# Performance work log

Hardware: AMD Instinct MI355X
Metric: run time of the kernel (lower is better)

Reference implementation:

```python
import jax, jax.numpy as jnp
import numpy as np

D_MODEL = 512
TOP_K = 4


def setup_inputs() -> dict:
    key = jax.random.key(0)
    ks = jax.random.split(key, 7)
    B, L, D = 16, 2048, D_MODEL
    s = 1.0 / np.sqrt(D)
    return {
        "x": jax.random.normal(ks[0], (B, L, D), dtype=jnp.float32),
        "Wq": jax.random.uniform(ks[1], (D, D), jnp.float32, -s, s),
        "bq": jax.random.uniform(ks[2], (D,), jnp.float32, -s, s),
        "Wk": jax.random.uniform(ks[3], (D, D), jnp.float32, -s, s),
        "bk": jax.random.uniform(ks[4], (D,), jnp.float32, -s, s),
        "Wv": jax.random.uniform(ks[5], (D, D), jnp.float32, -s, s),
        "bv": jax.random.uniform(ks[6], (D,), jnp.float32, -s, s),
    }


def reference(x, Wq, bq, Wk, bk, Wv, bv):
    B, L, D = x.shape
    # Linear projections (torch Linear: x @ W.T + b)
    Q = jnp.einsum('bld,ed->ble', x, Wq) + bq
    K = jnp.einsum('bld,ed->ble', x, Wk) + bk
    V = jnp.einsum('bld,ed->ble', x, Wv) + bv
    # FFT autocorrelation along time axis
    q_fft = jnp.fft.rfft(Q, axis=1)
    k_fft = jnp.fft.rfft(K, axis=1)
    corr = jnp.fft.irfft(q_fft * jnp.conj(k_fft), n=L, axis=1)  # [B, L, D]
    mean_corr = corr.mean(axis=-1)                               # [B, L]
    topk_vals, topk_idx = jax.lax.top_k(mean_corr, TOP_K)        # [B, K]
    weights = jax.nn.softmax(topk_vals, axis=-1)                 # [B, K]
    # torch.roll(V[b], shifts=lag, dims=0): out[t] = V[b, (t - lag) % L]
    t = jnp.arange(L)
    gather_idx = (t[None, None, :] - topk_idx[:, :, None]) % L   # [B, K, L]
    rolled = V[jnp.arange(B)[:, None, None], gather_idx]         # [B, K, L, D]
    agg = jnp.einsum('bk,bkld->bld', weights, rolled)
    return agg
```

## Files before the change

kernel.cpp:

```cpp
#include <hip/hip_runtime.h>
#include <math.h>

typedef unsigned short u16;
typedef unsigned int   u32;
typedef __attribute__((ext_vector_type(8))) __bf16 bf16x8;
typedef __attribute__((ext_vector_type(4))) float  f32x4;

#define BB 16
#define LL 2048
#define DD 512
#define NF 1025
#define TOPK 4

static const size_t OFF_XB  = 0;
static const size_t OFF_XTB = OFF_XB  + 8388608;
static const size_t OFF_GTB = OFF_XTB + 8388608;
static const size_t OFF_XC  = OFF_GTB + 8388608;
static const size_t OFF_BBM = OFF_XC  + 8388608;
static const size_t OFF_S   = OFF_BBM + 262144;
static const size_t OFF_W   = OFF_S   + (size_t)BB * NF * 2;
static const size_t OFF_I   = OFF_W   + BB * TOPK;

__device__ __forceinline__ u16 f2bf(float f) {
    u32 u = __float_as_uint(f);
    return (u16)((u + 0x7fffu + ((u >> 16) & 1u)) >> 16);
}
__device__ __forceinline__ float bf2f(u16 h) {
    return __uint_as_float(((u32)h) << 16);
}
__device__ __forceinline__ void gload16(const void* g, void* l) {
    __builtin_amdgcn_global_load_lds((const __attribute__((address_space(1))) void*)g,
                                     (__attribute__((address_space(3))) void*)l, 16, 0, 0);
}
__device__ __forceinline__ float2 cmul(float2 u, float2 v) {
    return make_float2(u.x * v.x - u.y * v.y, u.x * v.y + u.y * v.x);
}
__device__ __forceinline__ float2 cadd(float2 u, float2 v) { return make_float2(u.x + v.x, u.y + v.y); }
__device__ __forceinline__ float2 csub(float2 u, float2 v) { return make_float2(u.x - v.x, u.y - v.y); }

template<int M, int SGN>
__device__ __forceinline__ void radix4(const float2* __restrict__ src,
                                       float2* __restrict__ dst,
                                       const float2* __restrict__ twl, int tid) {
#pragma unroll
    for (int r = 0; r < 2; r++) {
        int w = tid + 256 * r;
        int k = w & (M - 1);
        int jm = w - k;
        float2 a = src[w], b = src[w + 512], c = src[w + 1024], d = src[w + 1536];
        float2 t0 = cadd(a, c), t1 = csub(a, c), t2 = cadd(b, d), bd = csub(b, d);
        float2 t3 = (SGN > 0) ? make_float2(bd.y, -bd.x)
                              : make_float2(-bd.y, bd.x);
        float2 T1 = twl[jm];
        float2 T2 = cmul(T1, T1);
        float2 T3 = cmul(T1, T2);
        int o = 4 * jm + k;
        dst[o]         = cadd(t0, t2);
        dst[o + M]     = cmul(cadd(t1, t3), T1);
        dst[o + 2 * M] = cmul(csub(t0, t2), T2);
        dst[o + 3 * M] = cmul(csub(t1, t3), T3);
    }
}

template<int SGN>
__device__ __forceinline__ void fft_r4_chain(float2* __restrict__ b1, float2* __restrict__ b2,
                                             const float2* __restrict__ twl, int tid) {
    radix4<2,   SGN>(b1, b2, twl, tid); __syncthreads();
    radix4<8,   SGN>(b2, b1, twl, tid); __syncthreads();
    radix4<32,  SGN>(b1, b2, twl, tid); __syncthreads();
    radix4<128, SGN>(b2, b1, twl, tid); __syncthreads();
    radix4<512, SGN>(b1, b2, twl, tid); __syncthreads();
}

__global__ __launch_bounds__(256) void k_pre(const float* __restrict__ x,
                                             const float* __restrict__ Wq,
                                             const float* __restrict__ Wk,
                                             const float* __restrict__ Wv,
                                             u16* __restrict__ xb,
                                             u16* __restrict__ xtb,
                                             u16* __restrict__ Bm,
                                             float* __restrict__ S) {
    __shared__ char sh[9216];
    int bid = blockIdx.x;
    int tid = threadIdx.x;
    if (bid < 64) {
        int g = bid;
        float (*As)[68] = (float(*)[68])sh;
        float (*Bs)[68] = (float(*)[68])(sh + 4352);
        int tx = tid & 15, ty = tid >> 4;
        int m0 = (g & 7) * 64, n0 = (g >> 3) * 64;
        float acc[4][4] = {};
        for (int k0 = 0; k0 < DD; k0 += 16) {
#pragma unroll
            for (int r = 0; r < 4; r++) {
                As[ty][tx + 16 * r] = Wq[(size_t)(k0 + ty) * DD + m0 + tx + 16 * r];
                Bs[ty][tx + 16 * r] = Wk[(size_t)(k0 + ty) * DD + n0 + tx + 16 * r];
            }
            __syncthreads();
#pragma unroll
            for (int k = 0; k < 16; k++) {
                float4 a4 = *(const float4*)&As[k][ty * 4];
                float4 b4 = *(const float4*)&Bs[k][tx * 4];
                float a[4] = {a4.x, a4.y, a4.z, a4.w};
                float b[4] = {b4.x, b4.y, b4.z, b4.w};
#pragma unroll
                for (int i = 0; i < 4; i++)
#pragma unroll
                    for (int j = 0; j < 4; j++) acc[i][j] += a[i] * b[j];
            }
            __syncthreads();
        }
#pragma unroll
        for (int i = 0; i < 4; i++) {
            uint2 o;
            o.x = (u32)f2bf(acc[i][0]) | ((u32)f2bf(acc[i][1]) << 16);
            o.y = (u32)f2bf(acc[i][2]) | ((u32)f2bf(acc[i][3]) << 16);
            *(uint2*)&Bm[(size_t)(m0 + ty * 4 + i) * DD + n0 + tx * 4] = o;
        }
    } else if (bid < 320) {
        int g = bid - 64;
        int i4 = g * 256 + tid;
        float4 w = ((const float4*)Wv)[i4];
        ushort4 o;
        o.x = f2bf(w.x); o.y = f2bf(w.y); o.z = f2bf(w.z); o.w = f2bf(w.w);
        ((ushort4*)(Bm + DD * DD))[i4] = o;
        if (i4 < 8200)
            ((float4*)S)[i4] = make_float4(0.f, 0.f, 0.f, 0.f);
    } else {
        int tb = bid - 320;
        int bx = tb & 7;
        int by = (tb >> 3) & 31;
        int bz = tb >> 8;
        u16 (*tile)[72] = (u16(*)[72])sh;
        int tx = tid & 15, ty = tid >> 4;
        int d0 = bx * 64, t0 = by * 64;
        const float* ip = x + ((size_t)bz * LL + t0) * DD + d0;
        u16* xbp = xb + ((size_t)bz * LL + t0) * DD + d0;
#pragma unroll
        for (int i = 0; i < 4; i++) {
            int r = ty + 16 * i;
            float4 v = *(const float4*)&ip[(size_t)r * DD + tx * 4];
            uint2 o;
            o.x = (u32)f2bf(v.x) | ((u32)f2bf(v.y) << 16);
            o.y = (u32)f2bf(v.z) | ((u32)f2bf(v.w) << 16);
            *(uint2*)&xbp[(size_t)r * DD + tx * 4] = o;
            tile[tx * 4 + 0][r] = (u16)(o.x);
            tile[tx * 4 + 1][r] = (u16)(o.x >> 16);
            tile[tx * 4 + 2][r] = (u16)(o.y);
            tile[tx * 4 + 3][r] = (u16)(o.y >> 16);
        }
        __syncthreads();
        u16* xtp = xtb + ((size_t)bz * DD + d0) * LL + t0;
#pragma unroll
        for (int i = 0; i < 2; i++) {
            int idx = tid + 256 * i;
            int dr = idx >> 3;
            int ch = idx & 7;
            uint4 o = *(const uint4*)&tile[dr][ch * 8];
            *(uint4*)&xtp[(size_t)dr * LL + ch * 8] = o;
        }
    }
}

__global__ __launch_bounds__(256, 2) void k_gemm2(const u16* __restrict__ Ab,
                                                  const u16* __restrict__ Bm,
                                                  u16* __restrict__ GTB) {
    __shared__ u16 smem[16384];
    u16* As = smem;
    u16* Bs = smem + 8192;
    int t = threadIdx.x;
    int wave = t >> 6, lane = t & 63;
    int l15 = lane & 15, l4 = lane >> 4;
    int qr = wave & 1, qc = wave >> 1;
    int m0 = blockIdx.x * 128, n0 = blockIdx.y * 128;

    f32x4 acc[4][4];
#pragma unroll
    for (int i = 0; i < 4; i++)
#pragma unroll
        for (int j = 0; j < 4; j++) acc[i][j] = (f32x4){0.f, 0.f, 0.f, 0.f};

    const u16* Ag = Ab + (size_t)m0 * DD;
    const u16* Bg = Bm + (size_t)n0 * DD;
    int a_base = (qr * 64 + l15) * 64 + l4 * 8;
    int b_base = (qc * 64 + l15) * 64 + l4 * 8;

    for (int k0 = 0; k0 < DD; k0 += 64) {
#pragma unroll
        for (int n = 0; n < 4; n++) {
            int c = wave * 256 + n * 64 + lane;
            int row = c >> 3, col = (c & 7) * 8;
            gload16(Ag + (size_t)row * DD + k0 + col, (char*)As + (size_t)(wave * 256 + n * 64) * 16);
            gload16(Bg + (size_t)row * DD + k0 + col, (char*)Bs + (size_t)(wave * 256 + n * 64) * 16);
        }
        __syncthreads();
#pragma unroll
        for (int kk = 0; kk < 64; kk += 32) {
            bf16x8 af[4], bq[4];
#pragma unroll
            for (int i = 0; i < 4; i++) af[i] = *(const bf16x8*)(As + a_base + i * 1024 + kk);
#pragma unroll
            for (int j = 0; j < 4; j++) bq[j] = *(const bf16x8*)(Bs + b_base + j * 1024 + kk);
#pragma unroll
            for (int i = 0; i < 4; i++)
#pragma unroll
                for (int j = 0; j < 4; j++)
                    acc[i][j] = __builtin_amdgcn_mfma_f32_16x16x32_bf16(af[i], bq[j], acc[i][j], 0, 0, 0);
        }
        __syncthreads();
    }

    float4* tb4 = (float4*)smem;
    int bidx = m0 >> 11;
    int tbase = m0 & 2047;
#pragma unroll
    for (int p = 0; p < 2; p++) {
        __syncthreads();
        if (qc == p) {
#pragma unroll
            for (int j = 0; j < 4; j++) {
                int nloc = j * 16 + l15;
#pragma unroll
                for (int i = 0; i < 4; i++) {
                    int tq = qr * 16 + i * 4 + l4;
                    tb4[nloc * 32 + (tq ^ (nloc & 31))] = *(float4*)&acc[i][j];
                }
            }
        }
        __syncthreads();
#pragma unroll
        for (int u = 0; u < 8; u++) {
            int idx4 = u * 256 + t;
            int nloc = idx4 >> 5, c4 = idx4 & 31;
            float4 v = tb4[nloc * 32 + (c4 ^ (nloc & 31))];
            uint2 o;
            o.x = (u32)f2bf(v.x) | ((u32)f2bf(v.y) << 16);
            o.y = (u32)f2bf(v.z) | ((u32)f2bf(v.w) << 16);
            *(uint2*)&GTB[((size_t)bidx * DD + n0 + p * 64 + nloc) * LL + tbase + c4 * 4] = o;
        }
    }
}

__global__ __launch_bounds__(256, 2) void k_gemm3(const u16* __restrict__ Ab,
                                                  const u16* __restrict__ Bm,
                                                  const float* __restrict__ bv,
                                                  float* __restrict__ out) {
    __shared__ u16 smem[16384];
    u16* As = smem;
    u16* Bs = smem + 8192;
    int t = threadIdx.x;
    int wave = t >> 6, lane = t & 63;
    int l15 = lane & 15, l4 = lane >> 4;
    int qr = wave & 1, qc = wave >> 1;
    int m0 = blockIdx.x * 128, n0 = blockIdx.y * 128;

    f32x4 acc[4][4];
#pragma unroll
    for (int i = 0; i < 4; i++)
#pragma unroll
        for (int j = 0; j < 4; j++) acc[i][j] = (f32x4){0.f, 0.f, 0.f, 0.f};

    const u16* Ag = Ab + (size_t)m0 * DD;
    const u16* Bg = Bm + (size_t)DD * DD + (size_t)n0 * DD;
    int a_base = (qr * 64 + l15) * 64 + l4 * 8;
    int b_base = (qc * 64 + l15) * 64 + l4 * 8;

    for (int k0 = 0; k0 < DD; k0 += 64) {
#pragma unroll
        for (int n = 0; n < 4; n++) {
            int c = wave * 256 + n * 64 + lane;
            int row = c >> 3, col = (c & 7) * 8;
            gload16(Ag + (size_t)row * DD + k0 + col, (char*)As + (size_t)(wave * 256 + n * 64) * 16);
            gload16(Bg + (size_t)row * DD + k0 + col, (char*)Bs + (size_t)(wave * 256 + n * 64) * 16);
        }
        __syncthreads();
#pragma unroll
        for (int kk = 0; kk < 64; kk += 32) {
            bf16x8 af[4], bq[4];
#pragma unroll
            for (int i = 0; i < 4; i++) af[i] = *(const bf16x8*)(As + a_base + i * 1024 + kk);
#pragma unroll
            for (int j = 0; j < 4; j++) bq[j] = *(const bf16x8*)(Bs + b_base + j * 1024 + kk);
#pragma unroll
            for (int i = 0; i < 4; i++)
#pragma unroll
                for (int j = 0; j < 4; j++)
                    acc[i][j] = __builtin_amdgcn_mfma_f32_16x16x32_bf16(af[i], bq[j], acc[i][j], 0, 0, 0);
        }
        __syncthreads();
    }

    float*  tb  = (float*)smem;
    float4* tb4 = (float4*)smem;
#pragma unroll
    for (int p = 0; p < 2; p++) {
        __syncthreads();
        if (qr == p) {
#pragma unroll
            for (int j = 0; j < 4; j++) {
                int nloc = qc * 64 + j * 16 + l15;
#pragma unroll
                for (int i = 0; i < 4; i++) {
#pragma unroll
                    for (int r = 0; r < 4; r++) {
                        int mloc = i * 16 + l4 * 4 + r;
                        int nc = ((nloc >> 2) ^ (mloc & 31)) << 2;
                        tb[mloc * 128 + nc + (nloc & 3)] = acc[i][j][r];
                    }
                }
            }
        }
        __syncthreads();
#pragma unroll
        for (int u = 0; u < 8; u++) {
            int idx4 = u * 256 + t;
            int mloc = idx4 >> 5, c4 = idx4 & 31;
            float4 v = tb4[mloc * 32 + (c4 ^ (mloc & 31))];
            float4 bias = *(const float4*)&bv[n0 + c4 * 4];
            v.x += bias.x; v.y += bias.y; v.z += bias.z; v.w += bias.w;
            *(float4*)&out[(size_t)(m0 + p * 64 + mloc) * DD + n0 + c4 * 4] = v;
        }
    }
}

__global__ __launch_bounds__(256) void k_fft(const u16* __restrict__ XTB,
                                             const u16* __restrict__ GTB,
                                             float* __restrict__ S) {
    __shared__ float2 lds[5120];
    float2* b1  = lds;
    float2* b2  = lds + 2048;
    float2* twl = lds + 4096;
    int tid = threadIdx.x;
    int grp = blockIdx.x;
    int b = blockIdx.y;
    for (int j = tid; j < 1024; j += 256) {
        float sn, cs;
        sincosf(-6.283185307179586f * (float)j / 2048.0f, &sn, &cs);
        twl[j] = make_float2(cs, sn);
    }
    __syncthreads();
    float2 sr[4];
#pragma unroll
    for (int r = 0; r < 4; r++) sr[r] = make_float2(0.f, 0.f);
    float2 s1024 = make_float2(0.f, 0.f);

    for (int c = 0; c < 8; c++) {
        int d = grp * 8 + c;
        const u16* xp = XTB + ((size_t)b * DD + d) * LL;
        const u16* gp = GTB + ((size_t)b * DD + d) * LL;
#pragma unroll
        for (int h = 0; h < 2; h++) {
            int j0 = 2 * tid + 512 * h;
            u32 xl = *(const u32*)&xp[j0];
            u32 xh = *(const u32*)&xp[j0 + 1024];
            u32 gl = *(const u32*)&gp[j0];
            u32 gh = *(const u32*)&gp[j0 + 1024];
            float2 a0 = make_float2(bf2f((u16)xl), bf2f((u16)gl));
            float2 a1 = make_float2(bf2f((u16)(xl >> 16)), bf2f((u16)(gl >> 16)));
            float2 c0 = make_float2(bf2f((u16)xh), bf2f((u16)gh));
            float2 c1 = make_float2(bf2f((u16)(xh >> 16)), bf2f((u16)(gh >> 16)));
            b1[2 * j0]     = cadd(a0, c0);
            b1[2 * j0 + 1] = cmul(csub(a0, c0), twl[j0]);
            b1[2 * j0 + 2] = cadd(a1, c1);
            b1[2 * j0 + 3] = cmul(csub(a1, c1), twl[j0 + 1]);
        }
        __syncthreads();
        fft_r4_chain<1>(b1, b2, twl, tid);
#pragma unroll
        for (int r = 0; r < 4; r++) {
            int f = tid + 256 * r;
            float2 p = b2[f];
            float2 q = b2[(2048 - f) & 2047];
            float ar = 0.5f * (p.x + q.x), ai = 0.5f * (p.y - q.y);
            float dr = p.x - q.x, di = p.y + q.y;
            float gr = 0.5f * di, gi = -0.5f * dr;
            sr[r].x += ar * gr + ai * gi;
            sr[r].y += ai * gr - ar * gi;
        }
        if (tid == 0) {
            float2 p = b2[1024];
            s1024.x += p.x * p.y;
        }
    }
    float* Sg = S + (size_t)b * NF * 2;
#pragma unroll
    for (int r = 0; r < 4; r++) {
        int f = tid + 256 * r;
        atomicAdd(&Sg[2 * f], sr[r].x);
        atomicAdd(&Sg[2 * f + 1], sr[r].y);
    }
    if (tid == 0) {
        atomicAdd(&Sg[2048], s1024.x);
        atomicAdd(&Sg[2049], s1024.y);
    }
}

__global__ __launch_bounds__(256) void k_topk(const float* __restrict__ S,
                                              float* __restrict__ wts,
                                              int* __restrict__ idxs) {
    __shared__ float2 lds[5120];
    float2* b1  = lds;
    float2* b2  = lds + 2048;
    float2* twl = lds + 4096;
    __shared__ float cv[2048];
    __shared__ float rv[256];
    __shared__ int ri[256];
    __shared__ float topv[TOPK];
    __shared__ int topi[TOPK];
    int tid = threadIdx.x;
    int b = blockIdx.x;
    const float* Sg = S + (size_t)b * NF * 2;
    for (int j = tid; j < 1024; j += 256) {
        float sn, cs;
        sincosf(6.283185307179586f * (float)j / 2048.0f, &sn, &cs);
        twl[j] = make_float2(cs, sn);
    }
    __syncthreads();
#pragma unroll
    for (int h = 0; h < 2; h++) {
        int j0 = 2 * tid + 512 * h;
#pragma unroll
        for (int e = 0; e < 2; e++) {
            int j = j0 + e;
            float2 zl = make_float2(Sg[2 * j], Sg[2 * j + 1]);
            int fh = j + 1024;
            int ms = 2048 - fh;
            float2 zh = (fh == 1024) ? make_float2(Sg[2048], Sg[2049])
                                     : make_float2(Sg[2 * ms], -Sg[2 * ms + 1]);
            b1[2 * j]     = cadd(zl, zh);
            b1[2 * j + 1] = cmul(csub(zl, zh), twl[j]);
        }
    }
    __syncthreads();
    fft_r4_chain<-1>(b1, b2, twl, tid);
    const float scale = 1.0f / ((float)LL * (float)DD);
    for (int f = tid; f < 2048; f += 256) cv[f] = b2[f].x * scale;
    __syncthreads();
    for (int r = 0; r < TOPK; r++) {
        float best = -3.0e38f;
        int bi = 0x7fffffff;
        for (int f = tid; f < 2048; f += 256) {
            bool taken = false;
            for (int q = 0; q < r; q++) taken |= (topi[q] == f);
            float v = cv[f];
            if (!taken && (v > best || (v == best && f < bi))) { best = v; bi = f; }
        }
        rv[tid] = best; ri[tid] = bi;
        __syncthreads();
        for (int s = 128; s > 0; s >>= 1) {
            if (tid < s) {
                float v2 = rv[tid + s]; int i2 = ri[tid + s];
                if (v2 > rv[tid] || (v2 == rv[tid] && i2 < ri[tid])) { rv[tid] = v2; ri[tid] = i2; }
            }
            __syncthreads();
        }
        if (tid == 0) { topv[r] = rv[0]; topi[r] = ri[0]; }
        __syncthreads();
    }
    if (tid == 0) {
        float mx = topv[0];
        float e[TOPK], sum = 0.f;
        for (int k = 0; k < TOPK; k++) { e[k] = expf(topv[k] - mx); sum += e[k]; }
        for (int k = 0; k < TOPK; k++) {
            wts[b * TOPK + k] = e[k] / sum;
            idxs[b * TOPK + k] = topi[k];
        }
    }
}

__global__ __launch_bounds__(128) void k_combine(const u16* __restrict__ XB,
                                                 const float* __restrict__ wts,
                                                 const int* __restrict__ idxs,
                                                 u16* __restrict__ XC) {
    int l = blockIdx.x, b = blockIdx.y;
    int t = threadIdx.x;
    const ushort4* Xb = (const ushort4*)(XB + (size_t)b * LL * DD);
    float4 acc = make_float4(0.f, 0.f, 0.f, 0.f);
#pragma unroll
    for (int k = 0; k < TOPK; k++) {
        float w = wts[b * TOPK + k];
        int r = (l - idxs[b * TOPK + k]) & (LL - 1);
        ushort4 v = Xb[(size_t)r * 128 + t];
        acc.x += w * bf2f(v.x); acc.y += w * bf2f(v.y);
        acc.z += w * bf2f(v.z); acc.w += w * bf2f(v.w);
    }
    ushort4 o;
    o.x = f2bf(acc.x); o.y = f2bf(acc.y); o.z = f2bf(acc.z); o.w = f2bf(acc.w);
    ((ushort4*)(XC + (size_t)b * LL * DD))[(size_t)l * 128 + t] = o;
}

extern "C" void kernel_launch(void* const* d_in, const int* in_sizes, int n_in,
                              void* d_out, int out_size, void* d_ws, size_t ws_size,
                              hipStream_t stream) {
    const float* x  = (const float*)d_in[0];
    const float* Wq = (const float*)d_in[1];
    const float* Wk = (const float*)d_in[3];
    const float* Wv = (const float*)d_in[5];
    const float* bv = (const float*)d_in[6];
    (void)in_sizes; (void)n_in; (void)out_size; (void)ws_size;

    float* ws  = (float*)d_ws;
    u16*   XB  = (u16*)(ws + OFF_XB);
    u16*   XTB = (u16*)(ws + OFF_XTB);
    u16*   GTB = (u16*)(ws + OFF_GTB);
    u16*   XC  = (u16*)(ws + OFF_XC);
    u16*   BM  = (u16*)(ws + OFF_BBM);
    float* S   = ws + OFF_S;
    float* wts = ws + OFF_W;
    int*   idx = (int*)(ws + OFF_I);
    float* out = (float*)d_out;

    k_pre<<<4416, 256, 0, stream>>>(x, Wq, Wk, Wv, XB, XTB, BM, S);
    k_gemm2<<<dim3((BB * LL) / 128, DD / 128), 256, 0, stream>>>(XB, BM, GTB);
    k_fft<<<dim3(64, BB), 256, 0, stream>>>(XTB, GTB, S);
    k_topk<<<BB, 256, 0, stream>>>(S, wts, idx);
    k_combine<<<dim3(LL, BB), 128, 0, stream>>>(XB, wts, idx, XC);
    k_gemm3<<<dim3((BB * LL) / 128, DD / 128), 256, 0, stream>>>(XC, BM, bv, out);
}
```

Baseline: 314.9 us.

## Pad FFT LDS buffers and keep per-stage twiddles in registers

Adds a padding index P(i)=i+i/32 to every LDS access in the radix-4 FFT stages to cut bank conflicts. It drops the shared twiddle table, instead computing per-thread, per-stage twiddles once into registers with sincosf, and skips the trivial twiddle multiplies in the last stage. The first butterfly pass is reorganized around wider uint2 loads with contiguous writes, and k_fft gets a launch bound asking for 4 blocks per CU. The cost is more registers and extra sincosf calls per thread.

```diff
diff --git a/kernel.cpp b/kernel.cpp
--- a/kernel.cpp
+++ b/kernel.cpp
@@ -38,38 +38,64 @@
 __device__ __forceinline__ float2 cadd(float2 u, float2 v) { return make_float2(u.x + v.x, u.y + v.y); }
 __device__ __forceinline__ float2 csub(float2 u, float2 v) { return make_float2(u.x - v.x, u.y - v.y); }
 
+__device__ __forceinline__ int P(int i) { return i + (i >> 5); }
+
 template<int M, int SGN>
 __device__ __forceinline__ void radix4(const float2* __restrict__ src,
                                        float2* __restrict__ dst,
-                                       const float2* __restrict__ twl, int tid) {
+                                       const float2* __restrict__ tw, int tid) {
 #pragma unroll
     for (int r = 0; r < 2; r++) {
         int w = tid + 256 * r;
         int k = w & (M - 1);
         int jm = w - k;
-        float2 a = src[w], b = src[w + 512], c = src[w + 1024], d = src[w + 1536];
+        float2 a = src[P(w)], b = src[P(w + 512)], c = src[P(w + 1024)], d = src[P(w + 1536)];
         float2 t0 = cadd(a, c), t1 = csub(a, c), t2 = cadd(b, d), bd = csub(b, d);
         float2 t3 = (SGN > 0) ? make_float2(bd.y, -bd.x)
                               : make_float2(-bd.y, bd.x);
-        float2 T1 = twl[jm];
-        float2 T2 = cmul(T1, T1);
-        float2 T3 = cmul(T1, T2);
         int o = 4 * jm + k;
-        dst[o]         = cadd(t0, t2);
-        dst[o + M]     = cmul(cadd(t1, t3), T1);
-        dst[o + 2 * M] = cmul(csub(t0, t2), T2);
-        dst[o + 3 * M] = cmul(csub(t1, t3), T3);
+        if (M == 512) {
+            dst[P(o)]         = cadd(t0, t2);
+            dst[P(o + M)]     = cadd(t1, t3);
+            dst[P(o + 2 * M)] = csub(t0, t2);
+            dst[P(o + 3 * M)] = csub(t1, t3);
+        } else {
+            float2 T1 = tw[r];
+            float2 T2 = cmul(T1, T1);
+            float2 T3 = cmul(T1, T2);
+            dst[P(o)]         = cadd(t0, t2);
+            dst[P(o + M)]     = cmul(cadd(t1, t3), T1);
+            dst[P(o + 2 * M)] = cmul(csub(t0, t2), T2);
+            dst[P(o + 3 * M)] = cmul(csub(t1, t3), T3);
+        }
     }
 }
 
 template<int SGN>
 __device__ __forceinline__ void fft_r4_chain(float2* __restrict__ b1, float2* __restrict__ b2,
-                                             const float2* __restrict__ twl, int tid) {
-    radix4<2,   SGN>(b1, b2, twl, tid); __syncthreads();
-    radix4<8,   SGN>(b2, b1, twl, tid); __syncthreads();
-    radix4<32,  SGN>(b1, b2, twl, tid); __syncthreads();
-    radix4<128, SGN>(b2, b1, twl, tid); __syncthreads();
-    radix4<512, SGN>(b1, b2, twl, tid); __syncthreads();
+                                             const float2 (*tws)[2], int tid) {
+    radix4<2,   SGN>(b1, b2, tws[0], tid); __syncthreads();
+    radix4<8,   SGN>(b2, b1, tws[1], tid); __syncthreads();
+    radix4<32,  SGN>(b1, b2, tws[2], tid); __syncthreads();
+    radix4<128, SGN>(b2, b1, tws[3], tid); __syncthreads();
+    radix4<512, SGN>(b1, b2, tws[4], tid); __syncthreads();
+}
+
+template<int SGN>
+__device__ __forceinline__ void make_tw(float2 tws[5][2], int tid) {
+    const float sc = (SGN > 0 ? -6.283185307179586f : 6.283185307179586f) / 2048.0f;
+#pragma unroll
+    for (int st = 0; st < 5; st++) {
+        int M = 2 << (2 * st);
+#pragma unroll
+        for (int r = 0; r < 2; r++) {
+            int w = tid + 256 * r;
+            int jm = w - (w & (M - 1));
+            float sn, cs;
+            sincosf(sc * (float)jm, &sn, &cs);
+            tws[st][r] = make_float2(cs, sn);
+        }
+    }
 }
 
 __global__ __launch_bounds__(256) void k_pre(const float* __restrict__ x,
@@ -323,54 +349,58 @@
     }
 }
 
-__global__ __launch_bounds__(256) void k_fft(const u16* __restrict__ XTB,
-                                             const u16* __restrict__ GTB,
-                                             float* __restrict__ S) {
-    __shared__ float2 lds[5120];
-    float2* b1  = lds;
-    float2* b2  = lds + 2048;
-    float2* twl = lds + 4096;
+__global__ __launch_bounds__(256, 4) void k_fft(const u16* __restrict__ XTB,
+                                                const u16* __restrict__ GTB,
+                                                float* __restrict__ S) {
+    __shared__ float2 lds[4224];
+    float2* b1 = lds;
+    float2* b2 = lds + 2112;
     int tid = threadIdx.x;
     int grp = blockIdx.x;
     int b = blockIdx.y;
-    for (int j = tid; j < 1024; j += 256) {
+
+    float2 tws[5][2];
+    make_tw<1>(tws, tid);
+    float2 tw2[4];
+#pragma unroll
+    for (int e = 0; e < 4; e++) {
         float sn, cs;
-        sincosf(-6.283185307179586f * (float)j / 2048.0f, &sn, &cs);
-        twl[j] = make_float2(cs, sn);
-    }
-    __syncthreads();
+        sincosf(-6.283185307179586f / 2048.0f * (float)(4 * tid + e), &sn, &cs);
+        tw2[e] = make_float2(cs, sn);
+    }
+
     float2 sr[4];
 #pragma unroll
     for (int r = 0; r < 4; r++) sr[r] = make_float2(0.f, 0.f);
-    float2 s1024 = make_float2(0.f, 0.f);
+    float s1024 = 0.f;
 
     for (int c = 0; c < 8; c++) {
         int d = grp * 8 + c;
         const u16* xp = XTB + ((size_t)b * DD + d) * LL;
         const u16* gp = GTB + ((size_t)b * DD + d) * LL;
-#pragma unroll
-        for (int h = 0; h < 2; h++) {
-            int j0 = 2 * tid + 512 * h;
-            u32 xl = *(const u32*)&xp[j0];
-            u32 xh = *(const u32*)&xp[j0 + 1024];
-            u32 gl = *(const u32*)&gp[j0];
-            u32 gh = *(const u32*)&gp[j0 + 1024];
-            float2 a0 = make_float2(bf2f((u16)xl), bf2f((u16)gl));
-            float2 a1 = make_float2(bf2f((u16)(xl >> 16)), bf2f((u16)(gl >> 16)));
-            float2 c0 = make_float2(bf2f((u16)xh), bf2f((u16)gh));
-            float2 c1 = make_float2(bf2f((u16)(xh >> 16)), bf2f((u16)(gh >> 16)));
-            b1[2 * j0]     = cadd(a0, c0);
-            b1[2 * j0 + 1] = cmul(csub(a0, c0), twl[j0]);
-            b1[2 * j0 + 2] = cadd(a1, c1);
-            b1[2 * j0 + 3] = cmul(csub(a1, c1), twl[j0 + 1]);
-        }
-        __syncthreads();
-        fft_r4_chain<1>(b1, b2, twl, tid);
+        int j0 = 4 * tid;
+        uint2 xl = *(const uint2*)&xp[j0];
+        uint2 xh = *(const uint2*)&xp[j0 + 1024];
+        uint2 gl = *(const uint2*)&gp[j0];
+        uint2 gh = *(const uint2*)&gp[j0 + 1024];
+        u32 xlw[2] = {xl.x, xl.y}, xhw[2] = {xh.x, xh.y};
+        u32 glw[2] = {gl.x, gl.y}, ghw[2] = {gh.x, gh.y};
+        float2* wp = &b1[P(8 * tid)];
+#pragma unroll
+        for (int e = 0; e < 4; e++) {
+            int sh = 16 * (e & 1);
+            float2 a0 = make_float2(bf2f((u16)(xlw[e >> 1] >> sh)), bf2f((u16)(glw[e >> 1] >> sh)));
+            float2 c0 = make_float2(bf2f((u16)(xhw[e >> 1] >> sh)), bf2f((u16)(ghw[e >> 1] >> sh)));
+            wp[2 * e]     = cadd(a0, c0);
+            wp[2 * e + 1] = cmul(csub(a0, c0), tw2[e]);
+        }
+        __syncthreads();
+        fft_r4_chain<1>(b1, b2, tws, tid);
 #pragma unroll
         for (int r = 0; r < 4; r++) {
             int f = tid + 256 * r;
-            float2 p = b2[f];
-            float2 q = b2[(2048 - f) & 2047];
+            float2 p = b2[P(f)];
+            float2 q = b2[P((2048 - f) & 2047)];
             float ar = 0.5f * (p.x + q.x), ai = 0.5f * (p.y - q.y);
             float dr = p.x - q.x, di = p.y + q.y;
             float gr = 0.5f * di, gi = -0.5f * dr;
@@ -378,8 +408,8 @@
             sr[r].y += ai * gr - ar * gi;
         }
         if (tid == 0) {
-            float2 p = b2[1024];
-            s1024.x += p.x * p.y;
+            float2 p = b2[P(1024)];
+            s1024 += p.x * p.y;
         }
     }
     float* Sg = S + (size_t)b * NF * 2;
@@ -390,18 +420,16 @@
         atomicAdd(&Sg[2 * f + 1], sr[r].y);
     }
     if (tid == 0) {
-        atomicAdd(&Sg[2048], s1024.x);
-        atomicAdd(&Sg[2049], s1024.y);
+        atomicAdd(&Sg[2048], s1024);
     }
 }
 
 __global__ __launch_bounds__(256) void k_topk(const float* __restrict__ S,
                                               float* __restrict__ wts,
                                               int* __restrict__ idxs) {
-    __shared__ float2 lds[5120];
-    float2* b1  = lds;
-    float2* b2  = lds + 2048;
-    float2* twl = lds + 4096;
+    __shared__ float2 lds[4224];
+    float2* b1 = lds;
+    float2* b2 = lds + 2112;
     __shared__ float cv[2048];
     __shared__ float rv[256];
     __shared__ int ri[256];
@@ -410,31 +438,31 @@
     int tid = threadIdx.x;
     int b = blockIdx.x;
     const float* Sg = S + (size_t)b * NF * 2;
-    for (int j = tid; j < 1024; j += 256) {
-        float sn, cs;
-        sincosf(6.283185307179586f * (float)j / 2048.0f, &sn, &cs);
-        twl[j] = make_float2(cs, sn);
-    }
-    __syncthreads();
+
+    float2 tws[5][2];
+    make_tw<-1>(tws, tid);
+
 #pragma unroll
     for (int h = 0; h < 2; h++) {
-        int j0 = 2 * tid + 512 * h;
 #pragma unroll
         for (int e = 0; e < 2; e++) {
-            int j = j0 + e;
+            int j = 2 * tid + 512 * h + e;
+            float sn, cs;
+            sincosf(6.283185307179586f / 2048.0f * (float)j, &sn, &cs);
+            float2 T = make_float2(cs, sn);
             float2 zl = make_float2(Sg[2 * j], Sg[2 * j + 1]);
             int fh = j + 1024;
             int ms = 2048 - fh;
             float2 zh = (fh == 1024) ? make_float2(Sg[2048], Sg[2049])
                                      : make_float2(Sg[2 * ms], -Sg[2 * ms + 1]);
-            b1[2 * j]     = cadd(zl, zh);
-            b1[2 * j + 1] = cmul(csub(zl, zh), twl[j]);
+            b1[P(2 * j)]     = cadd(zl, zh);
+            b1[P(2 * j + 1)] = cmul(csub(zl, zh), T);
         }
     }
     __syncthreads();
-    fft_r4_chain<-1>(b1, b2, twl, tid);
+    fft_r4_chain<-1>(b1, b2, tws, tid);
     const float scale = 1.0f / ((float)LL * (float)DD);
-    for (int f = tid; f < 2048; f += 256) cv[f] = b2[f].x * scale;
+    for (int f = tid; f < 2048; f += 256) cv[f] = b2[P(f)].x * scale;
     __syncthreads();
     for (int r = 0; r < TOPK; r++) {
         float best = -3.0e38f;
```

Result: slower. 358.5 us (+13.9%).
